# Kernel tuning notes

Measured on AMD Instinct MI355X. Metric: run time of the kernel, lower is better.

The kernel has to match this reference:

```python
import jax, jax.numpy as jnp
import numpy as np

HIDDEN = 1024
N_HEADS = 16
HEAD_DIM = HIDDEN // N_HEADS  # 64


def setup_inputs() -> dict:
    key = jax.random.key(0)
    ks = jax.random.split(key, 5)
    B, S = 4, 4096
    x = jax.random.normal(ks[0], (B, S, HIDDEN), dtype=jnp.float32)
    scale = 1.0 / np.sqrt(HIDDEN)
    wq = jax.random.normal(ks[1], (HIDDEN, HIDDEN), dtype=jnp.float32) * scale
    wk = jax.random.normal(ks[2], (HIDDEN, HIDDEN), dtype=jnp.float32) * scale
    wv = jax.random.normal(ks[3], (HIDDEN, HIDDEN), dtype=jnp.float32) * scale
    wo = jax.random.normal(ks[4], (HIDDEN, HIDDEN), dtype=jnp.float32) * scale
    return {"x": x, "wq": wq, "wk": wk, "wv": wv, "wo": wo}


def reference(x, wq, wk, wv, wo):
    # Weights stored as (out, in) like torch nn.Linear; y = x @ W^T
    B, S, H = x.shape
    q = (x @ wq.T).reshape(B, S, N_HEADS, HEAD_DIM)
    k = (x @ wk.T).reshape(B, S, N_HEADS, HEAD_DIM)
    v = (x @ wv.T).reshape(B, S, N_HEADS, HEAD_DIM)
    # Faithful to original: no transpose to (B,H,S,D) -> scores are over HEADS
    # attn: (B, S, H_heads, H_heads)
    attn = jnp.einsum("bshd,bsgd->bshg", q, k) / np.sqrt(HEAD_DIM)
    attn = jax.nn.softmax(attn, axis=-1)
    out = jnp.einsum("bshg,bsgd->bshd", attn, v).reshape(B, S, H)
    return out @ wo.T
```

## Files before the change

kernel.cpp:

```cpp
#include <hip/hip_runtime.h>
#include <hip/hip_bf16.h>


typedef __bf16 bf16;
typedef __attribute__((ext_vector_type(8))) __bf16 bf16x8;
typedef __attribute__((ext_vector_type(4))) float floatx4;

#define HIDDEN 1024
#define BM 128
#define BN 128
#define BK 32

#define FENCE() asm volatile("" ::: "memory")
#define BAR()                                                                  \
    do {                                                                       \
        FENCE();                                                               \
        __builtin_amdgcn_s_barrier();                                          \
        FENCE();                                                               \
    } while (0)
#define VMCNT(N) asm volatile("s_waitcnt vmcnt(" #N ")" ::: "memory")

__device__ __forceinline__ void async_load16(const bf16* g, bf16* lds) {
    __builtin_amdgcn_global_load_lds(
        (const __attribute__((address_space(1))) void*)g,
        (__attribute__((address_space(3))) void*)lds, 16, 0, 0);
}

__device__ __forceinline__ bf16x8 load8(const bf16* p) {
    return *(const bf16x8*)p;
}
__device__ __forceinline__ bf16x8 load8(const float* p) {
    floatx4 lo = *(const floatx4*)p;
    floatx4 hi = *(const floatx4*)(p + 4);
    bf16x8 r;
#pragma unroll
    for (int i = 0; i < 4; ++i) { r[i] = (bf16)lo[i]; r[i + 4] = (bf16)hi[i]; }
    return r;
}

__global__ __launch_bounds__(256) void cvt_all(
    const float* __restrict__ x,
    const float* __restrict__ wq, const float* __restrict__ wk,
    const float* __restrict__ wv, const float* __restrict__ wo,
    bf16* __restrict__ xb, bf16* __restrict__ wpk, int mh8)
{
    const int per = (HIDDEN * HIDDEN) / 8;
    int i = blockIdx.x * 256 + threadIdx.x;
    if (i < mh8) {
        *(bf16x8*)&xb[(size_t)i * 8] = load8(&x[(size_t)i * 8]);
    } else {
        int j = i - mh8;
        int wsel = j / per;
        int off  = (j - wsel * per) * 8;
        const float* s = wsel == 0 ? wq : wsel == 1 ? wk : wsel == 2 ? wv : wo;
        *(bf16x8*)&wpk[(size_t)j * 8] = load8(&s[off]);
    }
}


template <int S>
__device__ __forceinline__ void stage_half(const bf16* __restrict__ gbase,
                                           int ld, int kt, bf16* lhalf,
                                           int h, int tid) {
#pragma unroll
    for (int j = 0; j < 2; ++j) {
        const int ci = j * 512 + tid;
        const int rr = ci >> 3;
        const int cs = (ci & 7) ^ (rr & 7);
        const int gr = h * S + (rr & (S - 1)) + (rr >> (S == 64 ? 6 : 5)) * (2 * S);
        async_load16(&gbase[(size_t)gr * ld + kt + cs * 8], &lhalf[ci * 8]);
    }
}

__device__ __forceinline__ void ld_a4(const bf16* h, int wm, int col, int quad,
                                      int cx, bf16x8* a) {
#pragma unroll
    for (int i = 0; i < 4; ++i) {
        const int rr = i * 16 + col + (wm << 6);
#pragma unroll
        for (int kk = 0; kk < 2; ++kk)
            a[i * 2 + kk] =
                *(const bf16x8*)&h[rr * 64 + (((kk << 2) + quad) ^ cx) * 8];
    }
}
__device__ __forceinline__ void ld_b2(const bf16* h, int wn, int col, int quad,
                                      int cx, bf16x8* b) {
#pragma unroll
    for (int j = 0; j < 2; ++j) {
        const int rr = j * 16 + col + (wn << 5);
#pragma unroll
        for (int kk = 0; kk < 2; ++kk)
            b[j * 2 + kk] =
                *(const bf16x8*)&h[rr * 64 + (((kk << 2) + quad) ^ cx) * 8];
    }
}

template <int H, int G>
__device__ __forceinline__ void mmq(floatx4 (&acc)[8][4], const bf16x8 (&a)[8],
                                    const bf16x8 (&bb)[4]) {
    __builtin_amdgcn_s_setprio(1);
#pragma unroll
    for (int i = 0; i < 4; ++i)
#pragma unroll
        for (int j = 0; j < 2; ++j)
#pragma unroll
            for (int kk = 0; kk < 2; ++kk)
                acc[H * 4 + i][G * 2 + j] =
                    __builtin_amdgcn_mfma_f32_16x16x32_bf16(
                        a[i * 2 + kk], bb[j * 2 + kk],
                        acc[H * 4 + i][G * 2 + j], 0, 0, 0);
    __builtin_amdgcn_s_setprio(0);
}

template <typename TC>
__global__ __launch_bounds__(512, 2) void gemm8p(
    const bf16* __restrict__ A, const bf16* __restrict__ W,
    TC* __restrict__ C, int K, int lda, int ldc)
{
    __shared__ __align__(16) bf16 sA[2][2][128 * 64];
    __shared__ __align__(16) bf16 sB[2][2][128 * 64];

    const int tid  = threadIdx.x;
    const int lane = tid & 63;
    const int w    = tid >> 6;
    const int wm   = w >> 2;
    const int wn   = w & 3;
    const int m0   = blockIdx.x * 256;
    const int n0   = blockIdx.y * 256;
    const int col  = lane & 15;
    const int quad = lane >> 4;
    const int cx   = col & 7;

    const bf16* Ab = A + (size_t)m0 * lda;
    const bf16* Wb = W + (size_t)n0 * K;

    floatx4 acc[8][4] = {};
    bf16x8 a[8], b0[4], b1[4];

    const int T = K / 64;

    stage_half<64>(Ab, lda, 0, sA[0][0], 0, tid);
    stage_half<32>(Wb, K,   0, sB[0][0], 0, tid);
    stage_half<32>(Wb, K,   0, sB[0][1], 1, tid);
    stage_half<64>(Ab, lda, 0, sA[0][1], 1, tid);
    if (T > 1) {
        stage_half<64>(Ab, lda, 64, sA[1][0], 0, tid);
        stage_half<32>(Wb, K,   64, sB[1][0], 0, tid);
        stage_half<32>(Wb, K,   64, sB[1][1], 1, tid);
        VMCNT(6);
    } else {
        VMCNT(0);
    }
    BAR();

    for (int t = 0; t < T; ++t) {
        const int b   = t & 1;
        const int kt1 = (t + 1) * 64;
        const int kt2 = (t + 2) * 64;

        ld_a4(sA[b][0], wm, col, quad, cx, a);
        ld_b2(sB[b][0], wn, col, quad, cx, b0);
        if (t + 1 < T) stage_half<64>(Ab, lda, kt1, sA[b ^ 1][1], 1, tid);
        VMCNT(8);
        BAR();
        mmq<0, 0>(acc, a, b0);
        BAR();

        ld_b2(sB[b][1], wn, col, quad, cx, b1);
        if (t + 2 < T) stage_half<64>(Ab, lda, kt2, sA[b][0], 0, tid);
        VMCNT(8);
        BAR();
        mmq<0, 1>(acc, a, b1);
        BAR();

        ld_a4(sA[b][1], wm, col, quad, cx, a);
        if (t + 2 < T) stage_half<32>(Wb, K, kt2, sB[b][0], 0, tid);
        VMCNT(8);
        BAR();
        mmq<1, 1>(acc, a, b1);
        BAR();

        if (t + 2 < T) stage_half<32>(Wb, K, kt2, sB[b][1], 1, tid);
        VMCNT(8);
        BAR();
        mmq<1, 0>(acc, a, b0);
        BAR();
    }

#pragma unroll
    for (int mi = 0; mi < 8; ++mi) {
#pragma unroll
        for (int r = 0; r < 4; ++r) {
            const int row = m0 + wm * 128 + mi * 16 + quad * 4 + r;
#pragma unroll
            for (int ni = 0; ni < 4; ++ni) {
                const int cc = n0 + wn * 64 + ni * 16 + col;
                C[(size_t)row * ldc + cc] = (TC)acc[mi][ni][r];
            }
        }
    }
}

template <typename TA, typename TB, typename TC>
__global__ __launch_bounds__(256, 2) void gemm_bt(
    const TA* __restrict__ A, const TB* __restrict__ W,
    TC* __restrict__ C, int M, int N, int K)
{
    __shared__ __align__(16) bf16 sA[BM * BK];
    __shared__ __align__(16) bf16 sB[BN * BK];

    const int tid  = threadIdx.x;
    const int lane = tid & 63;
    const int w    = tid >> 6;
    const int wm   = w >> 1;
    const int wn   = w & 1;
    const int m0   = blockIdx.x * BM;
    const int n0   = blockIdx.y * BN;
    const int col  = lane & 15;
    const int quad = lane >> 4;

    floatx4 acc[4][4] = {};

    for (int kt = 0; kt < K; kt += BK) {
        bf16x8 ga[2], gb[2];
#pragma unroll
        for (int i = 0; i < 2; ++i) {
            const int c   = i * 256 + tid;
            const int row = c >> 2;
            const int kc  = c & 3;
            ga[i] = load8(&A[(size_t)(m0 + row) * K + kt + kc * 8]);
            gb[i] = load8(&W[(size_t)(n0 + row) * K + kt + kc * 8]);
        }
        __syncthreads();
#pragma unroll
        for (int i = 0; i < 2; ++i) {
            const int c = i * 256 + tid;
            *(bf16x8*)&sA[c * 8] = ga[i];
            *(bf16x8*)&sB[c * 8] = gb[i];
        }
        __syncthreads();

        bf16x8 af[4], bfr[4];
#pragma unroll
        for (int mi = 0; mi < 4; ++mi)
            af[mi] = *(const bf16x8*)&sA[(wm * 64 + mi * 16 + col) * BK + quad * 8];
#pragma unroll
        for (int ni = 0; ni < 4; ++ni)
            bfr[ni] = *(const bf16x8*)&sB[(wn * 64 + ni * 16 + col) * BK + quad * 8];

#pragma unroll
        for (int mi = 0; mi < 4; ++mi)
#pragma unroll
            for (int ni = 0; ni < 4; ++ni)
                acc[mi][ni] = __builtin_amdgcn_mfma_f32_16x16x32_bf16(
                    af[mi], bfr[ni], acc[mi][ni], 0, 0, 0);
    }

#pragma unroll
    for (int mi = 0; mi < 4; ++mi) {
#pragma unroll
        for (int r = 0; r < 4; ++r) {
            const int row = m0 + wm * 64 + mi * 16 + quad * 4 + r;
#pragma unroll
            for (int ni = 0; ni < 4; ++ni) {
                const int cc = n0 + wn * 64 + ni * 16 + col;
                C[(size_t)row * N + cc] = (TC)acc[mi][ni][r];
            }
        }
    }
}

__global__ __launch_bounds__(256) void attn_heads(
    bf16* base, size_t koff, size_t voff, int stride, bf16* ob)
{
    __shared__ __align__(16) bf16 sP[4][16 * 40];
    __shared__ __align__(16) bf16 sVt[4][64 * 40];

    const int tid   = threadIdx.x;
    const int lane  = tid & 63;
    const int w     = tid >> 6;
    const int token = blockIdx.x * 4 + w;
    const int col   = lane & 15;
    const int quad  = lane >> 4;

    bf16* qt = base + (size_t)token * stride;
    const bf16* kt = qt + koff;
    const bf16* vt = qt + voff;
    bf16* ot = ob + (size_t)token * HIDDEN;

    const bf16x8 z = {};
    *(bf16x8*)&sVt[w][lane * 40 + 16] = z;
    *(bf16x8*)&sVt[w][lane * 40 + 24] = z;
    if (lane < 16) {
        *(bf16x8*)&sP[w][lane * 40 + 16] = z;
        *(bf16x8*)&sP[w][lane * 40 + 24] = z;
    }

    bf16x8 qa0 = *(const bf16x8*)&qt[col * 64 + quad * 8];
    bf16x8 qa1 = *(const bf16x8*)&qt[col * 64 + 32 + quad * 8];
    bf16x8 kb0 = *(const bf16x8*)&kt[col * 64 + quad * 8];
    bf16x8 kb1 = *(const bf16x8*)&kt[col * 64 + 32 + quad * 8];
    floatx4 s = {};
    s = __builtin_amdgcn_mfma_f32_16x16x32_bf16(qa0, kb0, s, 0, 0, 0);
    s = __builtin_amdgcn_mfma_f32_16x16x32_bf16(qa1, kb1, s, 0, 0, 0);

    bf16x8 vc0, vc1;
#pragma unroll
    for (int j = 0; j < 8; ++j)  vc0[j] = vt[j * 64 + lane];
#pragma unroll
    for (int j = 0; j < 8; ++j)  vc1[j] = vt[(j + 8) * 64 + lane];
    *(bf16x8*)&sVt[w][lane * 40]     = vc0;
    *(bf16x8*)&sVt[w][lane * 40 + 8] = vc1;

#pragma unroll
    for (int r = 0; r < 4; ++r) {
        float x = s[r] * 0.125f;
        float m = x;
#pragma unroll
        for (int off = 1; off < 16; off <<= 1)
            m = fmaxf(m, __shfl_xor(m, off));
        float e = __expf(x - m);
        float su = e;
#pragma unroll
        for (int off = 1; off < 16; off <<= 1)
            su += __shfl_xor(su, off);
        sP[w][(quad * 4 + r) * 40 + col] = (bf16)(e / su);
    }

    bf16x8 pa = *(const bf16x8*)&sP[w][col * 40 + quad * 8];
#pragma unroll
    for (int dt = 0; dt < 4; ++dt) {
        bf16x8 vb = *(const bf16x8*)&sVt[w][(dt * 16 + col) * 40 + quad * 8];
        floatx4 o4 = {};
        o4 = __builtin_amdgcn_mfma_f32_16x16x32_bf16(pa, vb, o4, 0, 0, 0);
#pragma unroll
        for (int r = 0; r < 4; ++r)
            ot[(quad * 4 + r) * 64 + dt * 16 + col] = (bf16)o4[r];
    }
}

extern "C" void kernel_launch(void* const* d_in, const int* in_sizes, int n_in,
                              void* d_out, int out_size, void* d_ws, size_t ws_size,
                              hipStream_t stream) {
    const float* x  = (const float*)d_in[0];
    const float* wq = (const float*)d_in[1];
    const float* wk = (const float*)d_in[2];
    const float* wv = (const float*)d_in[3];
    const float* wo = (const float*)d_in[4];
    float* out = (float*)d_out;

    const int M = in_sizes[0] / HIDDEN;
    const size_t MH = (size_t)M * HIDDEN;
    const size_t WH = (size_t)HIDDEN * HIDDEN;

    const size_t need = (MH + 4 * WH + (size_t)M * 3 * HIDDEN) * sizeof(bf16);

    if (ws_size >= need && (M % 256) == 0) {
        bf16* xb  = (bf16*)d_ws;
        bf16* wpk = xb + MH;
        bf16* qkv = wpk + 4 * WH;

        const int mh8 = (int)(MH / 8);
        const int nchunks = mh8 + (int)(4 * WH / 8);
        cvt_all<<<dim3(nchunks / 256), 256, 0, stream>>>(x, wq, wk, wv, wo,
                                                         xb, wpk, mh8);

        gemm8p<bf16><<<dim3(M / 256, 3 * HIDDEN / 256), 512, 0, stream>>>(
            xb, wpk, qkv, HIDDEN, HIDDEN, 3 * HIDDEN);

        attn_heads<<<dim3(M / 4), 256, 0, stream>>>(qkv, 1024, 2048,
                                                    3 * HIDDEN, xb);

        gemm8p<float><<<dim3(M / 256, HIDDEN / 256), 512, 0, stream>>>(
            xb, wpk + 3 * WH, out, HIDDEN, HIDDEN, HIDDEN);
    } else {
        bf16* qb = (bf16*)d_ws;
        bf16* kb = qb + MH;
        bf16* vb = kb + MH;
        dim3 grid(M / BM, HIDDEN / BN), block(256);
        gemm_bt<float, float, bf16><<<grid, block, 0, stream>>>(x, wq, qb, M, HIDDEN, HIDDEN);
        gemm_bt<float, float, bf16><<<grid, block, 0, stream>>>(x, wk, kb, M, HIDDEN, HIDDEN);
        gemm_bt<float, float, bf16><<<grid, block, 0, stream>>>(x, wv, vb, M, HIDDEN, HIDDEN);
        attn_heads<<<dim3(M / 4), block, 0, stream>>>(qb, MH, 2 * MH, HIDDEN, qb);
        gemm_bt<bf16, float, float><<<grid, block, 0, stream>>>(qb, wo, out, M, HIDDEN, HIDDEN);
    }
}
```

Before: 288.5 us.

## Stage per-token Q/K/V into swizzled LDS via async loads in head attention

The head-attention kernel now copies each token's Q, K and V rows into a swizzled LDS buffer with async global-to-LDS loads, replacing strided scalar global reads of V. It computes P·V as V^T·P so the output is transposed in LDS and written back with coalesced 8-byte stores. The softmax max-subtraction is removed, which assumes the scaled scores stay small enough not to overflow exp. The GEMM tail also waits for all outstanding loads on the final iteration.

```diff
diff --git a/kernel.cpp b/kernel.cpp
--- a/kernel.cpp
+++ b/kernel.cpp
@@ -174,14 +174,20 @@
         BAR();
 
         ld_a4(sA[b][1], wm, col, quad, cx, a);
-        if (t + 2 < T) stage_half<32>(Wb, K, kt2, sB[b][0], 0, tid);
+        if (t + 2 < T) {
+            stage_half<32>(Wb, K, kt2, sB[b][0], 0, tid);
+        }
         VMCNT(8);
         BAR();
         mmq<1, 1>(acc, a, b1);
         BAR();
 
-        if (t + 2 < T) stage_half<32>(Wb, K, kt2, sB[b][1], 1, tid);
-        VMCNT(8);
+        if (t + 2 < T) {
+            stage_half<32>(Wb, K, kt2, sB[b][1], 1, tid);
+            VMCNT(8);
+        } else {
+            VMCNT(0);
+        }
         BAR();
         mmq<1, 0>(acc, a, b0);
         BAR();
@@ -273,8 +279,9 @@
 __global__ __launch_bounds__(256) void attn_heads(
     bf16* base, size_t koff, size_t voff, int stride, bf16* ob)
 {
+    __shared__ __align__(16) bf16 sQ[4][3072];
     __shared__ __align__(16) bf16 sP[4][16 * 40];
-    __shared__ __align__(16) bf16 sVt[4][64 * 40];
+    __shared__ __align__(16) bf16 sO[4][1024];
 
     const int tid   = threadIdx.x;
     const int lane  = tid & 63;
@@ -284,42 +291,48 @@
     const int quad  = lane >> 4;
 
     bf16* qt = base + (size_t)token * stride;
-    const bf16* kt = qt + koff;
-    const bf16* vt = qt + voff;
+    const bf16* src0 = qt;
+    const bf16* src1 = qt + koff;
+    const bf16* src2 = qt + voff;
     bf16* ot = ob + (size_t)token * HIDDEN;
 
-    const bf16x8 z = {};
-    *(bf16x8*)&sVt[w][lane * 40 + 16] = z;
-    *(bf16x8*)&sVt[w][lane * 40 + 24] = z;
-    if (lane < 16) {
-        *(bf16x8*)&sP[w][lane * 40 + 16] = z;
-        *(bf16x8*)&sP[w][lane * 40 + 24] = z;
-    }
-
-    bf16x8 qa0 = *(const bf16x8*)&qt[col * 64 + quad * 8];
-    bf16x8 qa1 = *(const bf16x8*)&qt[col * 64 + 32 + quad * 8];
-    bf16x8 kb0 = *(const bf16x8*)&kt[col * 64 + quad * 8];
-    bf16x8 kb1 = *(const bf16x8*)&kt[col * 64 + 32 + quad * 8];
+#pragma unroll
+    for (int i = 0; i < 6; ++i) {
+        const int ci = i * 64 + lane;
+        const int rl = (ci >> 3) & 15;
+        const int cs = (ci & 7) ^ (rl & 7);
+        const bf16* s = (i < 2) ? src0 : (i < 4) ? src1 : src2;
+        async_load16(&s[(rl * 8 + cs) * 8], &sQ[w][ci * 8]);
+    }
+    VMCNT(0);
+
+    bf16x8 qa[2], kb[2];
+#pragma unroll
+    for (int kk = 0; kk < 2; ++kk) {
+        const int c = ((kk << 2) + quad) ^ (col & 7);
+        qa[kk] = *(const bf16x8*)&sQ[w][(col * 8 + c) * 8];
+        kb[kk] = *(const bf16x8*)&sQ[w][((16 + col) * 8 + c) * 8];
+    }
     floatx4 s = {};
-    s = __builtin_amdgcn_mfma_f32_16x16x32_bf16(qa0, kb0, s, 0, 0, 0);
-    s = __builtin_amdgcn_mfma_f32_16x16x32_bf16(qa1, kb1, s, 0, 0, 0);
-
-    bf16x8 vc0, vc1;
-#pragma unroll
-    for (int j = 0; j < 8; ++j)  vc0[j] = vt[j * 64 + lane];
-#pragma unroll
-    for (int j = 0; j < 8; ++j)  vc1[j] = vt[(j + 8) * 64 + lane];
-    *(bf16x8*)&sVt[w][lane * 40]     = vc0;
-    *(bf16x8*)&sVt[w][lane * 40 + 8] = vc1;
+    s = __builtin_amdgcn_mfma_f32_16x16x32_bf16(qa[0], kb[0], s, 0, 0, 0);
+    s = __builtin_amdgcn_mfma_f32_16x16x32_bf16(qa[1], kb[1], s, 0, 0, 0);
+
+    bf16x8 va[4] = {};
+    if (quad < 2) {
+#pragma unroll
+        for (int dt = 0; dt < 4; ++dt) {
+            const int cb = dt * 2 + (col >> 3);
+#pragma unroll
+            for (int j = 0; j < 8; ++j) {
+                const int r = 32 + quad * 8 + j;
+                va[dt][j] = sQ[w][(r * 8 + (cb ^ j)) * 8 + (col & 7)];
+            }
+        }
+    }
 
 #pragma unroll
     for (int r = 0; r < 4; ++r) {
-        float x = s[r] * 0.125f;
-        float m = x;
-#pragma unroll
-        for (int off = 1; off < 16; off <<= 1)
-            m = fmaxf(m, __shfl_xor(m, off));
-        float e = __expf(x - m);
+        float e = __expf(s[r] * 0.125f);
         float su = e;
 #pragma unroll
         for (int off = 1; off < 16; off <<= 1)
@@ -327,15 +340,25 @@
         sP[w][(quad * 4 + r) * 40 + col] = (bf16)(e / su);
     }
 
-    bf16x8 pa = *(const bf16x8*)&sP[w][col * 40 + quad * 8];
+    bf16x8 pa = {};
+    if (quad < 2) pa = *(const bf16x8*)&sP[w][col * 40 + quad * 8];
 #pragma unroll
     for (int dt = 0; dt < 4; ++dt) {
-        bf16x8 vb = *(const bf16x8*)&sVt[w][(dt * 16 + col) * 40 + quad * 8];
         floatx4 o4 = {};
-        o4 = __builtin_amdgcn_mfma_f32_16x16x32_bf16(pa, vb, o4, 0, 0, 0);
-#pragma unroll
-        for (int r = 0; r < 4; ++r)
-            ot[(quad * 4 + r) * 64 + dt * 16 + col] = (bf16)o4[r];
+        o4 = __builtin_amdgcn_mfma_f32_16x16x32_bf16(va[dt], pa, o4, 0, 0, 0);
+        union { bf16 h4[4]; uint2 u; } pk;
+#pragma unroll
+        for (int r = 0; r < 4; ++r) pk.h4[r] = (bf16)o4[r];
+        const int c8 = dt * 4 + quad;
+        *(uint2*)&sO[w][(col * 16 + (c8 ^ col)) * 4] = pk.u;
+    }
+
+#pragma unroll
+    for (int it = 0; it < 4; ++it) {
+        const int n8 = it * 64 + lane;
+        const int h = n8 >> 4, c8 = n8 & 15;
+        const uint2 d = *(const uint2*)&sO[w][(h * 16 + (c8 ^ h)) * 4];
+        *(uint2*)&ot[n8 * 4] = d;
     }
 }
 
```

Result: no change. 290.7 us (+0.7%).
